# Kernel tuning notes

Measured on AMD Instinct MI355X. Metric: run time of the kernel, lower is better.

## Reference

```python
import jax, jax.numpy as jnp
import numpy as np

B, C, H, W = 2, 1024, 64, 64
R, E, HE, T, K = 16, 4, 512, 3, 2


def setup_inputs() -> dict:
    key = jax.random.key(0)
    ks = jax.random.split(key, 12)
    s = 0.02
    return {
        "x": jax.random.normal(ks[0], (B, C, H, W), jnp.float32),
        "t": jax.random.normal(ks[1], (B, C, H, W), jnp.float32),
        "fc_w": jax.random.normal(ks[2], (C, 2 * C), jnp.float32) * s,
        "ln_g": jnp.ones((C,), jnp.float32),
        "ln_b": jnp.zeros((C,), jnp.float32),
        "f1_w1": jax.random.normal(ks[3], (C // R, C), jnp.float32) * s,
        "f1_b1": jnp.zeros((C // R,), jnp.float32),
        "f1_wa": jax.random.normal(ks[4], (C, C // R), jnp.float32) * s,
        "f1_ba": jnp.zeros((C,), jnp.float32),
        "f1_wb": jax.random.normal(ks[5], (C, C // R), jnp.float32) * s,
        "f1_bb": jnp.zeros((C,), jnp.float32),
        "w_gate": jax.random.normal(ks[6], (T, C, E), jnp.float32) * s,
        "e_w1": jax.random.normal(ks[7], (E, C, HE), jnp.float32) * s,
        "e_b1": jnp.zeros((E, HE), jnp.float32),
        "e_w2": jax.random.normal(ks[8], (E, HE, C), jnp.float32) * s,
        "e_b2": jnp.zeros((E, C), jnp.float32),
        "task_index": 1,
    }


def _cv_squared(v):
    eps = 1e-10
    return jnp.var(v, ddof=1) / (jnp.mean(v) ** 2 + eps)


def reference(x, t, fc_w, ln_g, ln_b, f1_w1, f1_b1, f1_wa, f1_ba, f1_wb, f1_bb,
              w_gate, e_w1, e_b1, e_w2, e_b2, task_index):
    b, c, h, w = x.shape
    n = h * w
    # MultiTaskGeneralFusion: SE-style dual-branch channel gating
    s = jnp.mean(x + t, axis=(2, 3))                        # [B, C]
    hid = jax.nn.relu(s @ f1_w1.T + f1_b1)                  # [B, C/r]
    a = hid @ f1_wa.T + f1_ba                               # [B, C]
    bb = hid @ f1_wb.T + f1_bb                              # [B, C]
    wts = jax.nn.softmax(jnp.stack([a, bb], axis=0), axis=0)  # [2, B, C]
    z = wts[0][:, :, None, None] * x + wts[1][:, :, None, None] * t
    # fused linear -> ReLU -> LayerNorm on concatenated tokens
    x3 = x.reshape(b, c, n).transpose(0, 2, 1)              # [B, N, C]
    t3 = t.reshape(b, c, n).transpose(0, 2, 1)
    y = jnp.concatenate([x3, t3], axis=-1)                  # [B, N, 2C]
    y = jax.nn.relu(jnp.einsum('bnd,cd->bnc', y, fc_w))     # [B, N, C]
    mu = jnp.mean(y, axis=-1, keepdims=True)
    var = jnp.mean((y - mu) ** 2, axis=-1, keepdims=True)
    y = (y - mu) * jax.lax.rsqrt(var + 1e-5) * ln_g + ln_b
    yf = y.reshape(b * n, c)                                # [BN, C]
    # MMoE top-k gating (eval mode: no gating noise)
    logits = yf @ w_gate[task_index]                        # [BN, E]
    top_logits, top_idx = jax.lax.top_k(logits, K)          # [BN, K]
    top_gates = jax.nn.softmax(top_logits, axis=-1)
    gates = jnp.zeros_like(logits).at[jnp.arange(b * n)[:, None], top_idx].set(top_gates)
    # dense expert compute, gated combine
    eh = jax.nn.relu(jnp.einsum('nc,ech->neh', yf, e_w1) + e_b1)   # [BN, E, HE]
    eo = jnp.einsum('neh,eho->neo', eh, e_w2) + e_b2               # [BN, E, C]
    ym = jnp.einsum('ne,neo->no', gates, eo)                        # [BN, C]
    importance = gates.sum(axis=0)
    load = (gates > 0).sum(axis=0).astype(jnp.float32)
    aux_loss = _cv_squared(importance) + _cv_squared(load)
    y4 = ym.reshape(b, n, c).transpose(0, 2, 1).reshape(b, c, h, w) + z
    return (y4, aux_loss)
```

## Files before the change

### kernel.cpp

```cpp
#include <hip/hip_runtime.h>
#include <cstddef>
#include <cstdint>

#define B_   2
#define C_   1024
#define N_   4096
#define M_   8192
#define K2_  2048
#define E_   4
#define HE_  512

typedef float f32x4 __attribute__((ext_vector_type(4)));
typedef short bf16x8 __attribute__((ext_vector_type(8)));
typedef _Float16 f16x8 __attribute__((ext_vector_type(8)));
typedef unsigned short u16x8 __attribute__((ext_vector_type(8)));

#define WAITV(N) asm volatile("s_waitcnt vmcnt(" #N ")" ::: "memory")
#define SBAR     __builtin_amdgcn_sched_barrier(0)

static __device__ __forceinline__ unsigned short f2bf(float f) {
  unsigned int u = __float_as_uint(f);
  u = u + 0x7fffu + ((u >> 16) & 1u);
  return (unsigned short)(u >> 16);
}
static __device__ __forceinline__ float bf2f(unsigned short h) {
  return __uint_as_float(((unsigned int)h) << 16);
}

static __device__ __forceinline__ void gl_lds16(const void* g, void* l) {
  __builtin_amdgcn_global_load_lds(
      (const __attribute__((address_space(1))) void*)(uintptr_t)g,
      (__attribute__((address_space(3))) void*)(unsigned)(uintptr_t)l,
      16, 0, 0);
}

__global__ __launch_bounds__(256) void k_se_gate(const float* __restrict__ s,
                                                 const float* __restrict__ w1, const float* __restrict__ b1,
                                                 const float* __restrict__ wa, const float* __restrict__ ba,
                                                 const float* __restrict__ wb, const float* __restrict__ bbv,
                                                 float* __restrict__ wts0) {
  __shared__ float hid[2][64];
  const int t = threadIdx.x;
  if (t < 128) {
    const int b = t >> 6, r = t & 63;
    float acc = b1[r];
    const float* sp = s + b * C_;
    const float* wp = w1 + r * C_;
    for (int c = 0; c < C_; ++c) acc = fmaf(sp[c], wp[c], acc);
    hid[b][r] = fmaxf(acc, 0.f);
  }
  __syncthreads();
  for (int o = t; o < B_ * C_; o += 256) {
    const int b = o >> 10, c = o & 1023;
    float a = ba[c], bb = bbv[c];
    #pragma unroll 8
    for (int r = 0; r < 64; ++r) {
      const float h = hid[b][r];
      a  = fmaf(h, wa[c * 64 + r], a);
      bb = fmaf(h, wb[c * 64 + r], bb);
    }
    wts0[o] = 1.f / (1.f + expf(bb - a));
  }
}

__global__ __launch_bounds__(256) void k_prep_act(const float* __restrict__ x,
                                                  const float* __restrict__ t,
                                                  _Float16* __restrict__ ah,
                                                  _Float16* __restrict__ am,
                                                  float* __restrict__ spart) {
  __shared__ float tile[64][65];
  const int c0 = blockIdx.x * 64, n0 = blockIdx.y * 64, b = blockIdx.z;
  const float* xb = x + (size_t)b * (C_ * N_);
  const float* tb = t + (size_t)b * (C_ * N_);
  _Float16* ahb = ah + (size_t)b * (N_ * (size_t)K2_);
  _Float16* amb = am + (size_t)b * (N_ * (size_t)K2_);
  const int tid = threadIdx.x;
  const int prow = tid >> 2, pseg = tid & 3;
  float psum = 0.f;
  #pragma unroll
  for (int srcsel = 0; srcsel < 2; ++srcsel) {
    const float* src = srcsel ? tb : xb;
    const int koff = srcsel ? C_ : 0;
    if (srcsel) __syncthreads();
    #pragma unroll
    for (int p = 0; p < 4; ++p) {
      const int f = tid + p * 256;
      const int cr = f >> 4, nq = f & 15;
      const float4 v = *(const float4*)(src + (size_t)(c0 + cr) * N_ + n0 + nq * 4);
      tile[cr][nq * 4 + 0] = v.x; tile[cr][nq * 4 + 1] = v.y;
      tile[cr][nq * 4 + 2] = v.z; tile[cr][nq * 4 + 3] = v.w;
    }
    __syncthreads();
    {
      float a = 0.f;
      #pragma unroll
      for (int u = 0; u < 16; ++u) a += tile[prow][pseg * 16 + u];
      psum += a;
    }
    #pragma unroll
    for (int p = 0; p < 2; ++p) {
      const int f = tid + p * 256;
      const int mr = f >> 3, kq = f & 7;
      f16x8 hv, mv;
      #pragma unroll
      for (int u = 0; u < 8; ++u) {
        const float v = tile[kq * 8 + u][mr] * 64.f;
        const _Float16 h = (_Float16)v;
        hv[u] = h;
        mv[u] = (_Float16)(v - (float)h);
      }
      const size_t off = (size_t)(n0 + mr) * K2_ + koff + c0 + kq * 8;
      *(f16x8*)(ahb + off) = hv;
      *(f16x8*)(amb + off) = mv;
    }
  }
  psum += __shfl_xor(psum, 1);
  psum += __shfl_xor(psum, 2);
  if (pseg == 0)
    spart[((size_t)(b * C_ + c0 + prow)) * 64 + blockIdx.y] = psum;
}

__global__ __launch_bounds__(256) void k_reduce2(const float* __restrict__ spart,
                                                 float* __restrict__ s) {
  const int idx = blockIdx.x * 256 + threadIdx.x;
  const float* p = spart + (size_t)idx * 64;
  float acc = 0.f;
  #pragma unroll
  for (int j = 0; j < 64; ++j) acc += p[j];
  s[idx] = acc * (1.f / (float)N_);
}

__global__ __launch_bounds__(256) void k_prep_fcw(const float* __restrict__ w,
                                                  _Float16* __restrict__ wh,
                                                  _Float16* __restrict__ wm) {
  const size_t i = ((size_t)blockIdx.x * 256 + threadIdx.x) * 8;
  const float4 v0 = *(const float4*)(w + i);
  const float4 v1 = *(const float4*)(w + i + 4);
  const float vv[8] = {v0.x, v0.y, v0.z, v0.w, v1.x, v1.y, v1.z, v1.w};
  f16x8 hv, mv;
  #pragma unroll
  for (int u = 0; u < 8; ++u) {
    const float sv = vv[u] * 4096.f;
    const _Float16 h = (_Float16)sv;
    hv[u] = h;
    mv[u] = (_Float16)(sv - (float)h);
  }
  *(f16x8*)(wh + i) = hv;
  *(f16x8*)(wm + i) = mv;
}

__global__ __launch_bounds__(256) void k_prep_tr(const float* __restrict__ src, long long zs, int srs,
                                                 unsigned short* __restrict__ dst, long long zo, int drs) {
  __shared__ float tile[64][65];
  const int c0 = blockIdx.x * 64, r0 = blockIdx.y * 64, z = blockIdx.z;
  const float* s = src + (size_t)z * zs;
  unsigned short* d = dst + (size_t)z * zo;
  const int tid = threadIdx.x;
  #pragma unroll
  for (int p = 0; p < 4; ++p) {
    const int f = tid + p * 256;
    const int rr = f >> 4, cq = f & 15;
    const float4 v = *(const float4*)(s + (size_t)(r0 + rr) * srs + c0 + cq * 4);
    tile[rr][cq * 4 + 0] = v.x; tile[rr][cq * 4 + 1] = v.y;
    tile[rr][cq * 4 + 2] = v.z; tile[rr][cq * 4 + 3] = v.w;
  }
  __syncthreads();
  #pragma unroll
  for (int p = 0; p < 2; ++p) {
    const int f = tid + p * 256;
    const int cr = f >> 3, rq = f & 7;
    u16x8 o;
    #pragma unroll
    for (int u = 0; u < 8; ++u) o[u] = f2bf(tile[rq * 8 + u][cr]);
    *(u16x8*)(d + (size_t)(c0 + cr) * drs + r0 + rq * 8) = o;
  }
}

__global__ __launch_bounds__(512, 2) void k_fc_mfma(const _Float16* __restrict__ Ah,
                                                    const _Float16* __restrict__ Am,
                                                    const _Float16* __restrict__ Bh,
                                                    const _Float16* __restrict__ Bm,
                                                    float* __restrict__ y) {
  __shared__ __align__(16) char lds[2][49152];
  const int tid = threadIdx.x, w = tid >> 6, l = tid & 63;
  const int flat = blockIdx.x + blockIdx.y * 8;
  const int swz = (flat & 7) * 32 + (flat >> 3);
  const int n0 = (swz & 7) * 128, m0 = (swz >> 3) * 256;
  const int wr = w >> 1, wc = w & 1, lg = l >> 4, lr = l & 15;
  f32x4 acc[4][4] = {};

  auto LDA = [&](char* bufb, const _Float16* src, int roff, int k0, int q) {
    const int chunk = q * 512 + tid;
    const int kg = chunk >> 8, row = chunk & 255;
    gl_lds16(src + (size_t)(m0 + row) * K2_ + k0 + kg * 8,
             bufb + roff + (q * 512 + w * 64) * 16);
  };
  auto LDB = [&](char* bufb, const _Float16* src, int roff, int k0) {
    const int kg = tid >> 7, row = tid & 127;
    gl_lds16(src + (size_t)(n0 + row) * K2_ + k0 + kg * 8,
             bufb + roff + (w * 64) * 16);
  };

  LDA(&lds[0][0], Ah, 0, 0, 0);
  LDA(&lds[0][0], Ah, 0, 0, 1);
  LDB(&lds[0][0], Bh, 32768, 0);
  LDB(&lds[0][0], Bm, 40960, 0);
  LDA(&lds[0][0], Am, 16384, 0, 0);
  LDA(&lds[0][0], Am, 16384, 0, 1);

  f16x8 a_h[4], b_h[4], b_m[4], a_m[4];
  for (int t = 0; t < 63; ++t) {
    const int cur = t & 1;
    const char* bb = &lds[cur][0];
    char* nb = &lds[cur ^ 1][0];
    const int nk = (t + 1) * 32;
    WAITV(3); SBAR;
    __builtin_amdgcn_s_barrier();
    LDA(nb, Ah, 0, nk, 0);
    LDA(nb, Ah, 0, nk, 1);
    #pragma unroll
    for (int i = 0; i < 4; ++i)
      a_h[i] = *(const f16x8*)(bb + (lg * 256 + wr * 64 + i * 16 + lr) * 16);
    #pragma unroll
    for (int j = 0; j < 4; ++j)
      b_h[j] = *(const f16x8*)(bb + 32768 + (lg * 128 + wc * 64 + j * 16 + lr) * 16);
    __builtin_amdgcn_s_setprio(1);
    #pragma unroll
    for (int i = 0; i < 4; ++i)
      #pragma unroll
      for (int j = 0; j < 4; ++j)
        acc[i][j] = __builtin_amdgcn_mfma_f32_16x16x32_f16(a_h[i], b_h[j], acc[i][j], 0, 0, 0);
    __builtin_amdgcn_s_setprio(0);
    WAITV(4); SBAR;
    __builtin_amdgcn_s_barrier();
    LDB(nb, Bh, 32768, nk);
    LDB(nb, Bm, 40960, nk);
    #pragma unroll
    for (int j = 0; j < 4; ++j)
      b_m[j] = *(const f16x8*)(bb + 40960 + (lg * 128 + wc * 64 + j * 16 + lr) * 16);
    __builtin_amdgcn_s_setprio(1);
    #pragma unroll
    for (int i = 0; i < 4; ++i)
      #pragma unroll
      for (int j = 0; j < 4; ++j)
        acc[i][j] = __builtin_amdgcn_mfma_f32_16x16x32_f16(a_h[i], b_m[j], acc[i][j], 0, 0, 0);
    __builtin_amdgcn_s_setprio(0);
    WAITV(4); SBAR;
    __builtin_amdgcn_s_barrier();
    LDA(nb, Am, 16384, nk, 0);
    LDA(nb, Am, 16384, nk, 1);
    #pragma unroll
    for (int i = 0; i < 4; ++i)
      a_m[i] = *(const f16x8*)(bb + 16384 + (lg * 256 + wr * 64 + i * 16 + lr) * 16);
    __builtin_amdgcn_s_setprio(1);
    #pragma unroll
    for (int i = 0; i < 4; ++i)
      #pragma unroll
      for (int j = 0; j < 4; ++j)
        acc[i][j] = __builtin_amdgcn_mfma_f32_16x16x32_f16(a_m[i], b_h[j], acc[i][j], 0, 0, 0);
    __builtin_amdgcn_s_setprio(0);
  }
  {
    const char* bb = &lds[1][0];
    WAITV(3); SBAR;
    __builtin_amdgcn_s_barrier();
    #pragma unroll
    for (int i = 0; i < 4; ++i)
      a_h[i] = *(const f16x8*)(bb + (lg * 256 + wr * 64 + i * 16 + lr) * 16);
    #pragma unroll
    for (int j = 0; j < 4; ++j)
      b_h[j] = *(const f16x8*)(bb + 32768 + (lg * 128 + wc * 64 + j * 16 + lr) * 16);
    #pragma unroll
    for (int i = 0; i < 4; ++i)
      #pragma unroll
      for (int j = 0; j < 4; ++j)
        acc[i][j] = __builtin_amdgcn_mfma_f32_16x16x32_f16(a_h[i], b_h[j], acc[i][j], 0, 0, 0);
    WAITV(2); SBAR;
    __builtin_amdgcn_s_barrier();
    #pragma unroll
    for (int j = 0; j < 4; ++j)
      b_m[j] = *(const f16x8*)(bb + 40960 + (lg * 128 + wc * 64 + j * 16 + lr) * 16);
    #pragma unroll
    for (int i = 0; i < 4; ++i)
      #pragma unroll
      for (int j = 0; j < 4; ++j)
        acc[i][j] = __builtin_amdgcn_mfma_f32_16x16x32_f16(a_h[i], b_m[j], acc[i][j], 0, 0, 0);
    WAITV(0); SBAR;
    __builtin_amdgcn_s_barrier();
    #pragma unroll
    for (int i = 0; i < 4; ++i)
      a_m[i] = *(const f16x8*)(bb + 16384 + (lg * 256 + wr * 64 + i * 16 + lr) * 16);
    #pragma unroll
    for (int i = 0; i < 4; ++i)
      #pragma unroll
      for (int j = 0; j < 4; ++j)
        acc[i][j] = __builtin_amdgcn_mfma_f32_16x16x32_f16(a_m[i], b_h[j], acc[i][j], 0, 0, 0);
  }
  #pragma unroll
  for (int i = 0; i < 4; ++i) {
    const int mb = m0 + wr * 64 + i * 16 + lg * 4;
    #pragma unroll
    for (int j = 0; j < 4; ++j) {
      const int n = n0 + wc * 64 + j * 16 + lr;
      #pragma unroll
      for (int r = 0; r < 4; ++r)
        y[(size_t)(mb + r) * C_ + n] = fmaxf(acc[i][j][r] * (1.f / 262144.f), 0.f);
    }
  }
}

__global__ __launch_bounds__(256) void k_ln_topk(const float* __restrict__ y,
                                                 const float* __restrict__ lng, const float* __restrict__ lnb,
                                                 const float* __restrict__ wg, const int* __restrict__ taskp,
                                                 unsigned short* __restrict__ yf, float* __restrict__ gates) {
  const int wv = threadIdx.x >> 6, ln = threadIdx.x & 63;
  const int m = blockIdx.x * 4 + wv;
  const float* yr = y + (size_t)m * C_;
  float4 v[4];
  #pragma unroll
  for (int ch = 0; ch < 4; ++ch) v[ch] = *(const float4*)(yr + ch * 256 + ln * 4);
  float sum = 0.f;
  #pragma unroll
  for (int ch = 0; ch < 4; ++ch) sum += (v[ch].x + v[ch].y) + (v[ch].z + v[ch].w);
  #pragma unroll
  for (int o = 32; o; o >>= 1) sum += __shfl_down(sum, o);
  sum = __shfl(sum, 0);
  const float mu = sum * (1.f / 1024.f);
  float q = 0.f;
  #pragma unroll
  for (int ch = 0; ch < 4; ++ch) {
    const float dx = v[ch].x - mu, dy = v[ch].y - mu, dz = v[ch].z - mu, dw = v[ch].w - mu;
    q += (dx * dx + dy * dy) + (dz * dz + dw * dw);
  }
  #pragma unroll
  for (int o = 32; o; o >>= 1) q += __shfl_down(q, o);
  q = __shfl(q, 0);
  const float rstd = rsqrtf(q * (1.f / 1024.f) + 1e-5f);
  const float* wrow = wg + (size_t)(*taskp) * (C_ * E_);
  float l0 = 0.f, l1 = 0.f, l2 = 0.f, l3 = 0.f;
  #pragma unroll
  for (int ch = 0; ch < 4; ++ch) {
    const int c = ch * 256 + ln * 4;
    const float4 gg = *(const float4*)(lng + c);
    const float4 bv = *(const float4*)(lnb + c);
    float f[4];
    f[0] = (v[ch].x - mu) * rstd * gg.x + bv.x;
    f[1] = (v[ch].y - mu) * rstd * gg.y + bv.y;
    f[2] = (v[ch].z - mu) * rstd * gg.z + bv.z;
    f[3] = (v[ch].w - mu) * rstd * gg.w + bv.w;
    uint2 pk;
    pk.x = (unsigned)f2bf(f[0]) | ((unsigned)f2bf(f[1]) << 16);
    pk.y = (unsigned)f2bf(f[2]) | ((unsigned)f2bf(f[3]) << 16);
    *(uint2*)(yf + (size_t)m * C_ + c) = pk;
    #pragma unroll
    for (int i = 0; i < 4; ++i) {
      const float4 we = *(const float4*)(wrow + (size_t)(c + i) * 4);
      l0 = fmaf(f[i], we.x, l0); l1 = fmaf(f[i], we.y, l1);
      l2 = fmaf(f[i], we.z, l2); l3 = fmaf(f[i], we.w, l3);
    }
  }
  #pragma unroll
  for (int o = 32; o; o >>= 1) {
    l0 += __shfl_down(l0, o); l1 += __shfl_down(l1, o);
    l2 += __shfl_down(l2, o); l3 += __shfl_down(l3, o);
  }
  if (ln == 0) {
    const float L[4] = {l0, l1, l2, l3};
    int i1 = 0; float best = L[0];
    #pragma unroll
    for (int e = 1; e < 4; ++e) if (L[e] > best) { best = L[e]; i1 = e; }
    int i2 = -1; float s2 = 0.f;
    #pragma unroll
    for (int e = 0; e < 4; ++e) if (e != i1 && (i2 < 0 || L[e] > s2)) { s2 = L[e]; i2 = e; }
    const float g1 = 1.f / (1.f + expf(s2 - best));
    const float g2 = 1.f - g1;
    float4 gv;
    gv.x = (i1 == 0) ? g1 : ((i2 == 0) ? g2 : 0.f);
    gv.y = (i1 == 1) ? g1 : ((i2 == 1) ? g2 : 0.f);
    gv.z = (i1 == 2) ? g1 : ((i2 == 2) ? g2 : 0.f);
    gv.w = (i1 == 3) ? g1 : ((i2 == 3) ? g2 : 0.f);
    *(float4*)(gates + (size_t)m * 4) = gv;
  }
}

__global__ __launch_bounds__(256) void k_sched(const float* __restrict__ gates,
                                               int* __restrict__ idx,
                                               int* __restrict__ pos4,
                                               int* __restrict__ meta) {
  __shared__ unsigned long long smask[4][128];
  __shared__ int scnt[4], sbase[4];
  const int w = threadIdx.x >> 6, lane = threadIdx.x & 63;
  {
    const int e = w;
    int cnt = 0;
    for (int it0 = 0; it0 < 128; it0 += 8) {
      float gv[8];
      #pragma unroll
      for (int u = 0; u < 8; ++u)
        gv[u] = gates[(size_t)((it0 + u) * 64 + lane) * 4 + e];
      #pragma unroll
      for (int u = 0; u < 8; ++u) {
        const unsigned long long mask = __ballot(gv[u] > 0.f);
        if (lane == 0) smask[e][it0 + u] = mask;
        cnt += (int)__popcll(mask);
      }
    }
    if (lane == 0) scnt[e] = cnt;
  }
  __syncthreads();
  if (threadIdx.x == 0) {
    int b = 0;
    for (int e = 0; e < 4; ++e) { sbase[e] = b; meta[e] = scnt[e]; meta[4 + e] = b; b += scnt[e]; }
    int nt = 0;
    for (int e = 0; e < 4; ++e)
      for (int k = 0; k < scnt[e]; k += 128) { meta[16 + 2 * nt] = e; meta[17 + 2 * nt] = k; ++nt; }
    meta[8] = nt;
  }
  __syncthreads();
  {
    const int e = w;
    int cnt = 0;
    const int b = sbase[e];
    for (int it = 0; it < 128; ++it) {
      const unsigned long long mask = smask[e][it];
      const int tok = it * 64 + lane;
      const bool act = (mask >> lane) & 1ull;
      const int pos = cnt + (int)__popcll(mask & ((1ull << lane) - 1ull));
      if (act) { idx[b + pos] = tok; pos4[(size_t)tok * 4 + e] = b + pos; }
      else pos4[(size_t)tok * 4 + e] = -1;
      cnt += (int)__popcll(mask);
    }
  }
}

__global__ __launch_bounds__(256) void k_moe1_mfma(const unsigned short* __restrict__ yf,
                                                   const short* __restrict__ Bw,
                                                   const float* __restrict__ b1,
                                                   const int* __restrict__ idx,
                                                   const int* __restrict__ meta,
                                                   unsigned short* __restrict__ eh) {
  __shared__ __align__(16) char lds[3][16384];
  const int tid = threadIdx.x, w = tid >> 6, l = tid & 63;
  if ((int)blockIdx.y >= meta[8]) return;
  const int e = meta[16 + 2 * blockIdx.y], rstart = meta[17 + 2 * blockIdx.y];
  const int cntE = meta[e], baseE = meta[4 + e];
  const int n0 = blockIdx.x * 128;
  const int wr = w >> 1, wc = w & 1, lg = l >> 4, lr = l & 15;
  f32x4 acc[4][4] = {};
  const int sg = tid >> 7, sr = tid & 127;
  const int rl = rstart + sr;
  const int tokA = idx[baseE + (rl < cntE ? rl : cntE - 1)];
  const size_t ga0 = (size_t)tokA * C_ + sg * 8;
  const size_t gb0 = (size_t)(e * HE_ + n0 + sr) * C_ + sg * 8;

  auto STAGE = [&](int buf, int k0) {
    char* b = &lds[buf][0] + w * 1024;
    gl_lds16(yf + ga0 + k0, b);
    gl_lds16(yf + ga0 + 16 + k0, b + 4096);
    gl_lds16(Bw + gb0 + k0, b + 8192);
    gl_lds16(Bw + gb0 + 16 + k0, b + 12288);
  };

  STAGE(0, 0);
  STAGE(1, 32);
  for (int it = 0; it < 32; ++it) {
    const int cur = it % 3;
    if (it < 31) { WAITV(4); } else { WAITV(0); }
    SBAR;
    __builtin_amdgcn_s_barrier();
    if (it < 30) STAGE((it + 2) % 3, (it + 2) * 32);
    const char* bb = &lds[cur][0];
    bf16x8 af[4], bfr[4];
    #pragma unroll
    for (int i = 0; i < 4; ++i)
      af[i] = *(const bf16x8*)(bb + lg * 2048 + (wr * 64 + i * 16 + lr) * 16);
    #pragma unroll
    for (int j = 0; j < 4; ++j)
      bfr[j] = *(const bf16x8*)(bb + 8192 + lg * 2048 + (wc * 64 + j * 16 + lr) * 16);
    __builtin_amdgcn_s_setprio(1);
    #pragma unroll
    for (int i = 0; i < 4; ++i)
      #pragma unroll
      for (int j = 0; j < 4; ++j)
        acc[i][j] = __builtin_amdgcn_mfma_f32_16x16x32_bf16(af[i], bfr[j], acc[i][j], 0, 0, 0);
    __builtin_amdgcn_s_setprio(0);
  }
  #pragma unroll
  for (int j = 0; j < 4; ++j) {
    const int col = n0 + wc * 64 + j * 16 + lr;
    const float bias = b1[e * HE_ + col];
    #pragma unroll
    for (int i = 0; i < 4; ++i) {
      const int mb = wr * 64 + i * 16 + lg * 4;
      #pragma unroll
      for (int r = 0; r < 4; ++r) {
        const int rr = rstart + mb + r;
        if (rr < cntE) {
          const float v = fmaxf(acc[i][j][r] + bias, 0.f);
          eh[(size_t)(baseE + rr) * HE_ + col] = f2bf(v);
        }
      }
    }
  }
}

__global__ __launch_bounds__(256) void k_moe2_mfma(const unsigned short* __restrict__ eh,
                                                   const short* __restrict__ Bw,
                                                   const float* __restrict__ b2,
                                                   const float* __restrict__ gates,
                                                   const int* __restrict__ idx,
                                                   const int* __restrict__ meta,
                                                   unsigned short* __restrict__ eo) {
  __shared__ __align__(16) char lds[3][16384];
  const int tid = threadIdx.x, w = tid >> 6, l = tid & 63;
  if ((int)blockIdx.y >= meta[8]) return;
  const int e = meta[16 + 2 * blockIdx.y], rstart = meta[17 + 2 * blockIdx.y];
  const int cntE = meta[e], baseE = meta[4 + e];
  const int n0 = blockIdx.x * 128;
  const int wr = w >> 1, wc = w & 1, lg = l >> 4, lr = l & 15;
  f32x4 acc[4][4] = {};
  const int sg = tid >> 7, sr = tid & 127;
  const size_t ga0 = (size_t)(baseE + rstart + sr) * HE_ + sg * 8;
  const size_t gb0 = (size_t)(n0 + sr) * K2_ + e * HE_ + sg * 8;

  auto STAGE = [&](int buf, int k0) {
    char* b = &lds[buf][0] + w * 1024;
    gl_lds16(eh + ga0 + k0, b);
    gl_lds16(eh + ga0 + 16 + k0, b + 4096);
    gl_lds16(Bw + gb0 + k0, b + 8192);
    gl_lds16(Bw + gb0 + 16 + k0, b + 12288);
  };

  STAGE(0, 0);
  STAGE(1, 32);
  for (int it = 0; it < 16; ++it) {
    const int cur = it % 3;
    if (it < 15) { WAITV(4); } else { WAITV(0); }
    SBAR;
    __builtin_amdgcn_s_barrier();
    if (it < 14) STAGE((it + 2) % 3, (it + 2) * 32);
    const char* bb = &lds[cur][0];
    bf16x8 af[4], bfr[4];
    #pragma unroll
    for (int i = 0; i < 4; ++i)
      af[i] = *(const bf16x8*)(bb + lg * 2048 + (wr * 64 + i * 16 + lr) * 16);
    #pragma unroll
    for (int j = 0; j < 4; ++j)
      bfr[j] = *(const bf16x8*)(bb + 8192 + lg * 2048 + (wc * 64 + j * 16 + lr) * 16);
    __builtin_amdgcn_s_setprio(1);
    #pragma unroll
    for (int i = 0; i < 4; ++i)
      #pragma unroll
      for (int j = 0; j < 4; ++j)
        acc[i][j] = __builtin_amdgcn_mfma_f32_16x16x32_bf16(af[i], bfr[j], acc[i][j], 0, 0, 0);
    __builtin_amdgcn_s_setprio(0);
  }
  #pragma unroll
  for (int i = 0; i < 4; ++i) {
    const int mb = wr * 64 + i * 16 + lg * 4;
    #pragma unroll
    for (int r = 0; r < 4; ++r) {
      const int rr = rstart + mb + r;
      if (rr < cntE) {
        const int tok = idx[baseE + rr];
        const float g = gates[(size_t)tok * 4 + e];
        #pragma unroll
        for (int j = 0; j < 4; ++j) {
          const int n = n0 + wc * 64 + j * 16 + lr;
          const float val = (acc[i][j][r] + b2[e * C_ + n]) * g;
          eo[(size_t)(baseE + rr) * C_ + n] = f2bf(val);
        }
      }
    }
  }
}

__global__ __launch_bounds__(256) void k_aux(const float* __restrict__ gates, float* __restrict__ outp) {
  const int t = threadIdx.x;
  float imp[4] = {0, 0, 0, 0}, ld[4] = {0, 0, 0, 0};
  for (int m = t; m < M_; m += 256) {
    const float4 g = *(const float4*)(gates + (size_t)m * 4);
    imp[0] += g.x; imp[1] += g.y; imp[2] += g.z; imp[3] += g.w;
    ld[0] += (g.x > 0.f) ? 1.f : 0.f; ld[1] += (g.y > 0.f) ? 1.f : 0.f;
    ld[2] += (g.z > 0.f) ? 1.f : 0.f; ld[3] += (g.w > 0.f) ? 1.f : 0.f;
  }
  __shared__ float red[8][4];
  const int wv = t >> 6, ln = t & 63;
  #pragma unroll
  for (int e = 0; e < 4; ++e) {
    float a = imp[e], b = ld[e];
    #pragma unroll
    for (int o = 32; o; o >>= 1) { a += __shfl_down(a, o); b += __shfl_down(b, o); }
    if (ln == 0) { red[e][wv] = a; red[4 + e][wv] = b; }
  }
  __syncthreads();
  if (t == 0) {
    float I[4], L[4];
    #pragma unroll
    for (int e = 0; e < 4; ++e) {
      I[e] = red[e][0] + red[e][1] + red[e][2] + red[e][3];
      L[e] = red[4 + e][0] + red[4 + e][1] + red[4 + e][2] + red[4 + e][3];
    }
    const float mi = (I[0] + I[1] + I[2] + I[3]) * 0.25f;
    const float vi = ((I[0] - mi) * (I[0] - mi) + (I[1] - mi) * (I[1] - mi) +
                      (I[2] - mi) * (I[2] - mi) + (I[3] - mi) * (I[3] - mi)) / 3.f;
    const float ml = (L[0] + L[1] + L[2] + L[3]) * 0.25f;
    const float vl = ((L[0] - ml) * (L[0] - ml) + (L[1] - ml) * (L[1] - ml) +
                      (L[2] - ml) * (L[2] - ml) + (L[3] - ml) * (L[3] - ml)) / 3.f;
    *outp = vi / (mi * mi + 1e-10f) + vl / (ml * ml + 1e-10f);
  }
}

__global__ __launch_bounds__(256) void k_final(const unsigned short* __restrict__ eo,
                                               const int* __restrict__ pos4,
                                               const float* __restrict__ x, const float* __restrict__ t,
                                               const float* __restrict__ wts0, float* __restrict__ out) {
  __shared__ float tile[64][65];
  const int c0 = blockIdx.x * 64, n0 = blockIdx.y * 64, b = blockIdx.z;
  const int tid = threadIdx.x;
  #pragma unroll
  for (int p = 0; p < 4; ++p) {
    const int f = tid + p * 256;
    const int row = f >> 4, cq = f & 15;
    const int m = b * N_ + n0 + row;
    const int4 pp = *(const int4*)(pos4 + (size_t)m * 4);
    float v0 = 0.f, v1 = 0.f, v2 = 0.f, v3 = 0.f;
    const int pa[4] = {pp.x, pp.y, pp.z, pp.w};
    #pragma unroll
    for (int e = 0; e < 4; ++e) {
      if (pa[e] >= 0) {
        const ushort4 u = *(const ushort4*)(eo + (size_t)pa[e] * C_ + c0 + cq * 4);
        v0 += bf2f(u.x); v1 += bf2f(u.y); v2 += bf2f(u.z); v3 += bf2f(u.w);
      }
    }
    tile[row][cq * 4 + 0] = v0; tile[row][cq * 4 + 1] = v1;
    tile[row][cq * 4 + 2] = v2; tile[row][cq * 4 + 3] = v3;
  }
  __syncthreads();
  #pragma unroll
  for (int p = 0; p < 4; ++p) {
    const int f = tid + p * 256;
    const int cr = f >> 4, nq = f & 15;
    const int c = c0 + cr;
    const float w0 = wts0[b * C_ + c];
    const float w1 = 1.f - w0;
    const size_t idx2 = (size_t)(b * C_ + c) * N_ + n0 + nq * 4;
    const float4 xv = *(const float4*)(x + idx2);
    const float4 tv = *(const float4*)(t + idx2);
    float4 o;
    o.x = tile[nq * 4 + 0][cr] + w0 * xv.x + w1 * tv.x;
    o.y = tile[nq * 4 + 1][cr] + w0 * xv.y + w1 * tv.y;
    o.z = tile[nq * 4 + 2][cr] + w0 * xv.z + w1 * tv.z;
    o.w = tile[nq * 4 + 3][cr] + w0 * xv.w + w1 * tv.w;
    *(float4*)(out + idx2) = o;
  }
}

extern "C" void kernel_launch(void* const* d_in, const int* in_sizes, int n_in,
                              void* d_out, int out_size, void* d_ws, size_t ws_size,
                              hipStream_t stream) {
  const float* x     = (const float*)d_in[0];
  const float* t     = (const float*)d_in[1];
  const float* fc_w  = (const float*)d_in[2];
  const float* ln_g  = (const float*)d_in[3];
  const float* ln_b  = (const float*)d_in[4];
  const float* f1_w1 = (const float*)d_in[5];
  const float* f1_b1 = (const float*)d_in[6];
  const float* f1_wa = (const float*)d_in[7];
  const float* f1_ba = (const float*)d_in[8];
  const float* f1_wb = (const float*)d_in[9];
  const float* f1_bb = (const float*)d_in[10];
  const float* w_gate = (const float*)d_in[11];
  const float* e_w1  = (const float*)d_in[12];
  const float* e_b1  = (const float*)d_in[13];
  const float* e_w2  = (const float*)d_in[14];
  const float* e_b2  = (const float*)d_in[15];
  const int*   task  = (const int*)d_in[16];
  float* out = (float*)d_out;

  char* ws = (char*)d_ws;
  float*          y     = (float*)ws;
  float*          spart = (float*)ws;
  unsigned short* eo    = (unsigned short*)ws;
  _Float16*       ah    = (_Float16*)(ws + 33554432);
  _Float16*       am    = (_Float16*)(ws + 67108864);
  unsigned short* yf    = (unsigned short*)(ws + 33554432);
  unsigned short* eh    = (unsigned short*)(ws + 50331648);
  int*            idx   = (int*)(ws + 67108864);
  int*            pos4  = (int*)(ws + 67174400);
  int*            meta  = (int*)(ws + 67305472);
  _Float16* wh  = (_Float16*)(ws + 100663296);
  _Float16* wm  = (_Float16*)(ws + 104857600);
  short*    w1t = (short*)(ws + 109051904);
  short*    w2t = (short*)(ws + 113246208);
  float* sbuf  = (float*)(ws + 117440512);
  float* wts0  = (float*)(ws + 117448704);
  float* gates = (float*)(ws + 117456896);

  k_prep_fcw<<<1024, 256, 0, stream>>>(fc_w, wh, wm);
  k_prep_tr<<<dim3(8, 16, 4), 256, 0, stream>>>(e_w1, 524288LL, 512, (unsigned short*)w1t, 524288LL, 1024);
  k_prep_tr<<<dim3(16, 8, 4), 256, 0, stream>>>(e_w2, 524288LL, 1024, (unsigned short*)w2t, 512LL, 2048);
  k_prep_act<<<dim3(16, 64, 2), 256, 0, stream>>>(x, t, ah, am, spart);
  k_reduce2<<<8, 256, 0, stream>>>(spart, sbuf);
  k_se_gate<<<1, 256, 0, stream>>>(sbuf, f1_w1, f1_b1, f1_wa, f1_ba, f1_wb, f1_bb, wts0);
  k_fc_mfma<<<dim3(8, 32), 512, 0, stream>>>(ah, am, wh, wm, y);
  k_ln_topk<<<M_ / 4, 256, 0, stream>>>(y, ln_g, ln_b, w_gate, task, yf, gates);
  k_sched<<<1, 256, 0, stream>>>(gates, idx, pos4, meta);
  k_moe1_mfma<<<dim3(4, 132), 256, 0, stream>>>(yf, w1t, e_b1, idx, meta, eh);
  k_moe2_mfma<<<dim3(8, 132), 256, 0, stream>>>(eh, w2t, e_b2, gates, idx, meta, eo);
  k_aux<<<1, 256, 0, stream>>>(gates, out + (size_t)B_ * C_ * N_);
  k_final<<<dim3(C_ / 64, N_ / 64, B_), 256, 0, stream>>>(eo, pos4, x, t, wts0, out);
}
```

Before: 413.5 us.

## Parallelize routing scan across waves and remap MoE GEMM blocks XCD-aware

The scheduling kernel now has every wave read float4 gate rows and ballot all four experts at once. A small per-expert prefix scan in shared memory replaces the serial per-wave loops, and pos4 is written with int4 stores. The two expert GEMM kernels remap the flat block index with an 8-way interleave so that neighbouring tiles sharing an expert's weights and tokens land on the same XCD, which should improve L2 reuse. The remap hardcodes grid sizes (66, 132), so it depends on a matching launch configuration.

```diff
diff --git a/kernel.cpp b/kernel.cpp
--- a/kernel.cpp
+++ b/kernel.cpp
@@ -388,48 +388,50 @@
                                                int* __restrict__ pos4,
                                                int* __restrict__ meta) {
   __shared__ unsigned long long smask[4][128];
-  __shared__ int scnt[4], sbase[4];
+  __shared__ int pref[4][129];
+  __shared__ int sbase[4];
   const int w = threadIdx.x >> 6, lane = threadIdx.x & 63;
-  {
-    const int e = w;
-    int cnt = 0;
-    for (int it0 = 0; it0 < 128; it0 += 8) {
-      float gv[8];
-      #pragma unroll
-      for (int u = 0; u < 8; ++u)
-        gv[u] = gates[(size_t)((it0 + u) * 64 + lane) * 4 + e];
-      #pragma unroll
-      for (int u = 0; u < 8; ++u) {
-        const unsigned long long mask = __ballot(gv[u] > 0.f);
-        if (lane == 0) smask[e][it0 + u] = mask;
-        cnt += (int)__popcll(mask);
-      }
-    }
-    if (lane == 0) scnt[e] = cnt;
+  for (int it = w; it < 128; it += 4) {
+    const float4 g = *(const float4*)(gates + (size_t)(it * 64 + lane) * 4);
+    const unsigned long long m0 = __ballot(g.x > 0.f);
+    const unsigned long long m1 = __ballot(g.y > 0.f);
+    const unsigned long long m2 = __ballot(g.z > 0.f);
+    const unsigned long long m3 = __ballot(g.w > 0.f);
+    if (lane == 0) { smask[0][it] = m0; smask[1][it] = m1; smask[2][it] = m2; smask[3][it] = m3; }
+  }
+  __syncthreads();
+  if (threadIdx.x < 4) {
+    const int e = threadIdx.x;
+    int run = 0;
+    for (int it = 0; it < 128; ++it) { pref[e][it] = run; run += (int)__popcll(smask[e][it]); }
+    pref[e][128] = run;
   }
   __syncthreads();
   if (threadIdx.x == 0) {
-    int b = 0;
-    for (int e = 0; e < 4; ++e) { sbase[e] = b; meta[e] = scnt[e]; meta[4 + e] = b; b += scnt[e]; }
-    int nt = 0;
-    for (int e = 0; e < 4; ++e)
-      for (int k = 0; k < scnt[e]; k += 128) { meta[16 + 2 * nt] = e; meta[17 + 2 * nt] = k; ++nt; }
+    int b = 0, nt = 0;
+    for (int e = 0; e < 4; ++e) {
+      const int c = pref[e][128];
+      meta[e] = c; meta[4 + e] = b; sbase[e] = b;
+      for (int k = 0; k < c; k += 128) { meta[16 + 2 * nt] = e; meta[17 + 2 * nt] = k; ++nt; }
+      b += c;
+    }
     meta[8] = nt;
   }
   __syncthreads();
-  {
-    const int e = w;
-    int cnt = 0;
-    const int b = sbase[e];
-    for (int it = 0; it < 128; ++it) {
+  for (int it = w; it < 128; it += 4) {
+    const int tok = it * 64 + lane;
+    int4 p4;
+    int pv[4];
+    #pragma unroll
+    for (int e = 0; e < 4; ++e) {
       const unsigned long long mask = smask[e][it];
-      const int tok = it * 64 + lane;
       const bool act = (mask >> lane) & 1ull;
-      const int pos = cnt + (int)__popcll(mask & ((1ull << lane) - 1ull));
-      if (act) { idx[b + pos] = tok; pos4[(size_t)tok * 4 + e] = b + pos; }
-      else pos4[(size_t)tok * 4 + e] = -1;
-      cnt += (int)__popcll(mask);
-    }
+      const int slot = sbase[e] + pref[e][it] + (int)__popcll(mask & ((1ull << lane) - 1ull));
+      if (act) idx[slot] = tok;
+      pv[e] = act ? slot : -1;
+    }
+    p4.x = pv[0]; p4.y = pv[1]; p4.z = pv[2]; p4.w = pv[3];
+    *(int4*)(pos4 + (size_t)tok * 4) = p4;
   }
 }
 
@@ -441,10 +443,13 @@
                                                    unsigned short* __restrict__ eh) {
   __shared__ __align__(16) char lds[3][16384];
   const int tid = threadIdx.x, w = tid >> 6, l = tid & 63;
-  if ((int)blockIdx.y >= meta[8]) return;
-  const int e = meta[16 + 2 * blockIdx.y], rstart = meta[17 + 2 * blockIdx.y];
+  const int flat = blockIdx.x + blockIdx.y * 4;
+  const int work = (flat & 7) * 66 + (flat >> 3);
+  const int tix = work >> 2, colb = work & 3;
+  if (tix >= meta[8]) return;
+  const int e = meta[16 + 2 * tix], rstart = meta[17 + 2 * tix];
   const int cntE = meta[e], baseE = meta[4 + e];
-  const int n0 = blockIdx.x * 128;
+  const int n0 = colb * 128;
   const int wr = w >> 1, wc = w & 1, lg = l >> 4, lr = l & 15;
   f32x4 acc[4][4] = {};
   const int sg = tid >> 7, sr = tid & 127;
@@ -513,10 +518,13 @@
                                                    unsigned short* __restrict__ eo) {
   __shared__ __align__(16) char lds[3][16384];
   const int tid = threadIdx.x, w = tid >> 6, l = tid & 63;
-  if ((int)blockIdx.y >= meta[8]) return;
-  const int e = meta[16 + 2 * blockIdx.y], rstart = meta[17 + 2 * blockIdx.y];
+  const int flat = blockIdx.x + blockIdx.y * 8;
+  const int work = (flat & 7) * 132 + (flat >> 3);
+  const int tix = work >> 3, colb = work & 7;
+  if (tix >= meta[8]) return;
+  const int e = meta[16 + 2 * tix], rstart = meta[17 + 2 * tix];
   const int cntE = meta[e], baseE = meta[4 + e];
-  const int n0 = blockIdx.x * 128;
+  const int n0 = colb * 128;
   const int wr = w >> 1, wc = w & 1, lg = l >> 4, lr = l & 15;
   f32x4 acc[4][4] = {};
   const int sg = tid >> 7, sr = tid & 127;
```

New measurement: 411.4 us. No clear change (-0.5%).
